# Kernel tuning notes

Measured on AMD Instinct MI355X. Metric: run time of the kernel, lower is better.

The kernel has to match this reference:

```python
import jax, jax.numpy as jnp
import numpy as np

D = 1024          # input_dim == output_dim (module requires this)
H = 4 * D         # expert hidden dim
E = 8             # num_experts
TOP_K = 2
N = 16384         # tokens


def setup_inputs() -> dict:
    key = jax.random.key(0)
    ks = jax.random.split(key, 8)
    s = 0.02
    return {
        "x": jax.random.normal(ks[0], (N, D), dtype=jnp.float32),
        "grad": jax.random.normal(ks[1], (N, 1), dtype=jnp.float32),
        "rW": jax.random.normal(ks[2], (D + 1, E), dtype=jnp.float32) * s,
        "rb": jnp.zeros((E,), dtype=jnp.float32),
        "W1": jax.random.normal(ks[3], (E, D, H), dtype=jnp.float32) * s,
        "b1": jnp.zeros((E, H), dtype=jnp.float32),
        "W2": jax.random.normal(ks[4], (E, H, D), dtype=jnp.float32) * s,
        "b2": jnp.zeros((E, D), dtype=jnp.float32),
    }


def reference(x, grad, rW, rb, W1, b1, W2, b2):
    # Router over [x, grad]
    logits = jnp.concatenate([x, grad], axis=-1) @ rW + rb          # [N, E]
    probs = jax.nn.softmax(logits, axis=-1)                          # [N, E]
    topk_probs, topk_idx = jax.lax.top_k(probs, TOP_K)               # [N, K]
    # Dense gate matrix: gate[n, e] = topk prob if e selected else 0
    gates = jnp.zeros_like(probs).at[jnp.arange(x.shape[0])[:, None], topk_idx].add(topk_probs)
    # Combine: out = sum_e gate_e * MLP_e(x). Dropout is identity at eval.
    out = jnp.zeros((x.shape[0], D), dtype=x.dtype)
    for e in range(E):  # fixed small loop over experts
        h = jax.nn.gelu(x @ W1[e] + b1[e], approximate=False)        # [N, H]
        y = h @ W2[e] + b2[e]                                        # [N, D]
        out = out + gates[:, e:e + 1] * y
    return out, probs
```

## Files before the change

kernel.cpp:

```cpp
#include <hip/hip_runtime.h>
#include <hip/hip_bf16.h>
#include <math.h>

#define NTOK 16384
#define DDIM 1024
#define HDIM 4096
#define NEXP 8

typedef __bf16 bf16_t;
typedef __bf16 bf16x8 __attribute__((ext_vector_type(8)));
typedef float f32x4 __attribute__((ext_vector_type(4)));

__device__ __forceinline__ void gld16(const bf16_t* g, bf16_t* l) {
    __builtin_amdgcn_global_load_lds(
        (const __attribute__((address_space(1))) void*)g,
        (__attribute__((address_space(3))) void*)l, 16, 0, 0);
}

__device__ __forceinline__ void stage_half(const bf16_t* __restrict__ g, int K, int kofs,
                                           bf16_t* l, int tid) {
#pragma unroll
    for (int c = 0; c < 2; ++c) {
        const int s = c * 512 + tid;
        const int kg = s >> 7, r = s & 127;
        gld16(g + (size_t)r * K + (kofs + kg * 8), l + (size_t)s * 8);
    }
}


__global__ void init_counts(int* counts) {
    if (threadIdx.x < NEXP) counts[threadIdx.x] = 0;
}

__global__ void router_kernel(const float* __restrict__ x, const float* __restrict__ grad,
                              const float* __restrict__ rW, const float* __restrict__ rb,
                              float* __restrict__ probs, int* __restrict__ t2i,
                              float* __restrict__ t2g, int* __restrict__ counts) {
    const int lane = threadIdx.x & 63;
    const int n = blockIdx.x * 4 + (threadIdx.x >> 6);
    float acc[NEXP];
#pragma unroll
    for (int e = 0; e < NEXP; ++e) acc[e] = 0.f;
    const float* xr = x + (size_t)n * DDIM;
    for (int d = lane; d < DDIM; d += 64) {
        float xv = xr[d];
        const float* rr = rW + (size_t)d * NEXP;
#pragma unroll
        for (int e = 0; e < NEXP; ++e) acc[e] = fmaf(xv, rr[e], acc[e]);
    }
#pragma unroll
    for (int e = 0; e < NEXP; ++e) {
#pragma unroll
        for (int off = 32; off > 0; off >>= 1)
            acc[e] += __shfl_xor(acc[e], off, 64);
    }
    if (lane == 0) {
        float gv = grad[n];
        float p[NEXP];
        float mx = -1e30f;
#pragma unroll
        for (int e = 0; e < NEXP; ++e) {
            p[e] = acc[e] + gv * rW[(size_t)DDIM * NEXP + e] + rb[e];
            mx = fmaxf(mx, p[e]);
        }
        float s = 0.f;
#pragma unroll
        for (int e = 0; e < NEXP; ++e) { p[e] = expf(p[e] - mx); s += p[e]; }
        float inv = 1.f / s;
        int i1 = 0; float v1 = -1.f;
#pragma unroll
        for (int e = 0; e < NEXP; ++e) {
            p[e] *= inv;
            probs[(size_t)n * NEXP + e] = p[e];
            if (p[e] > v1) { v1 = p[e]; i1 = e; }
        }
        int i2 = 0; float v2 = -2.f;
#pragma unroll
        for (int e = 0; e < NEXP; ++e) {
            if (e != i1 && p[e] > v2) { v2 = p[e]; i2 = e; }
        }
        t2i[n * 2] = i1; t2i[n * 2 + 1] = i2;
        t2g[n * 2] = v1; t2g[n * 2 + 1] = v2;
        atomicAdd(&counts[i1], 1);
        atomicAdd(&counts[i2], 1);
    }
}

__global__ void offsets_kernel(const int* __restrict__ counts, int* __restrict__ offsets,
                               int* __restrict__ cursor) {
    if (threadIdx.x == 0) {
        int s = 0;
        for (int e = 0; e < NEXP; ++e) { offsets[e] = s; cursor[e] = s; s += counts[e]; }
    }
}

__global__ void build_lists(const int* __restrict__ t2i, const float* __restrict__ t2g,
                            int* __restrict__ cursor, int* __restrict__ tok,
                            float* __restrict__ gate, int* __restrict__ tslot) {
    int n = blockIdx.x * 256 + threadIdx.x;
#pragma unroll
    for (int k = 0; k < 2; ++k) {
        int e = t2i[n * 2 + k];
        int slot = atomicAdd(&cursor[e], 1);
        tok[slot] = n;
        gate[slot] = t2g[n * 2 + k];
        tslot[n * 2 + k] = slot;
    }
}

__global__ void gather_kernel(const float* __restrict__ x, const int* __restrict__ tok,
                              bf16_t* __restrict__ Xg) {
    const int r = blockIdx.x;
    const int t = threadIdx.x;
    const int token = tok[r];
    float4 v = ((const float4*)(x + (size_t)token * DDIM))[t];
    bf16_t o[4] = { (bf16_t)v.x, (bf16_t)v.y, (bf16_t)v.z, (bf16_t)v.w };
    *(uint2*)(Xg + (size_t)r * DDIM + t * 4) = *(const uint2*)o;
}

__global__ void transpose_cast(const float* __restrict__ in, bf16_t* __restrict__ out,
                               int R, int C) {
    __shared__ float tile[32][33];
    const size_t ebase = (size_t)blockIdx.z * R * C;
    const int c0 = blockIdx.x * 32, r0 = blockIdx.y * 32;
    const int tx = threadIdx.x, ty = threadIdx.y;
#pragma unroll
    for (int j = 0; j < 32; j += 8)
        tile[ty + j][tx] = in[ebase + (size_t)(r0 + ty + j) * C + c0 + tx];
    __syncthreads();
#pragma unroll
    for (int j = 0; j < 32; j += 8)
        out[ebase + (size_t)(c0 + ty + j) * R + r0 + tx] = (bf16_t)tile[tx][ty + j];
}

__global__ void combine_kernel(const float* __restrict__ Yg, const int* __restrict__ tslot,
                               float* __restrict__ out) {
    const int n = blockIdx.x, t = threadIdx.x;
    const int s1 = tslot[n * 2], s2 = tslot[n * 2 + 1];
    const float4 a = ((const float4*)(Yg + (size_t)s1 * DDIM))[t];
    const float4 b = ((const float4*)(Yg + (size_t)s2 * DDIM))[t];
    ((float4*)(out + (size_t)n * DDIM))[t] =
        make_float4(a.x + b.x, a.y + b.y, a.z + b.z, a.w + b.w);
}

#define PHASE_SYNC() do { \
    __builtin_amdgcn_s_barrier(); \
    asm volatile("s_waitcnt lgkmcnt(0)" ::: "memory"); \
    __builtin_amdgcn_sched_barrier(0); \
    __builtin_amdgcn_s_setprio(1); \
} while (0)

#define PHASE_END() do { \
    __builtin_amdgcn_s_setprio(0); \
    __builtin_amdgcn_s_barrier(); \
} while (0)

#define MMA16(QA, QB) do { \
    _Pragma("unroll") \
    for (int mt = 0; mt < 4; ++mt) { \
        _Pragma("unroll") \
        for (int nt = 0; nt < 2; ++nt) { \
            _Pragma("unroll") \
            for (int ks = 0; ks < 2; ++ks) \
                acc[(QA) * 4 + mt][(QB) * 2 + nt] = \
                    __builtin_amdgcn_mfma_f32_16x16x32_bf16( \
                        aF[mt][ks], bF[nt][ks], acc[(QA) * 4 + mt][(QB) * 2 + nt], 0, 0, 0); \
        } \
    } \
} while (0)

template <int K, int EPI>
__global__ __launch_bounds__(512, 2)
void moe_gemm8(const bf16_t* __restrict__ A, const bf16_t* __restrict__ B,
               const float* __restrict__ bias, bf16_t* __restrict__ Hout,
               float* __restrict__ Yg, const int* __restrict__ counts,
               const int* __restrict__ offsets, const float* __restrict__ gate,
               int gx) {
    const int NT = K / 64;
    const int nwg = gridDim.x;
    const int q8 = nwg >> 3;
    const int v = (blockIdx.x & 7) * q8 + (blockIdx.x >> 3);
    const int per_e = gx * 64;
    const int e = v / per_e;
    const int rem = v - e * per_e;
    const int xsc = gx >> 2;
    const int sup = rem >> 5, sub = rem & 31;
    const int ys = sup / xsc, xs = sup - ys * xsc;
    const int yb = ys * 8 + (sub >> 2), xb = xs * 4 + (sub & 3);

    const int count = counts[e];
    const int m0 = yb * 256;
    if (m0 >= count) return;
    const int n0 = xb * 256;
    const int off = offsets[e];

    const bf16_t* Ae = A + (size_t)(off + m0) * K;
    const bf16_t* Be = B + (size_t)e * HDIM * DDIM + (size_t)n0 * K;
    const bf16_t* Ae1 = Ae + (size_t)128 * K;
    const bf16_t* Be1 = Be + (size_t)128 * K;

    __shared__ __align__(16) bf16_t lds[2][2][2][8192];

    const int tid = threadIdx.x;
    const int lane = tid & 63;
    const int lm = lane & 15, hi = lane >> 4;
    const int wv = tid >> 6;
    const int wm16 = (wv >> 2) << 4;
    const int wn16 = (wv & 3) << 4;

    f32x4 acc[8][4];
    const f32x4 zf = {0.f, 0.f, 0.f, 0.f};
#pragma unroll
    for (int i = 0; i < 8; ++i)
#pragma unroll
        for (int j = 0; j < 4; ++j) acc[i][j] = zf;

    bf16x8 aF[4][2], bF[2][2];
    auto readA = [&](const bf16_t* Ab) {
#pragma unroll
        for (int mt = 0; mt < 4; ++mt)
#pragma unroll
            for (int ks = 0; ks < 2; ++ks)
                aF[mt][ks] = *(const bf16x8*)(Ab + (size_t)((ks * 4 + hi) * 128 +
                                                            mt * 32 + wm16 + lm) * 8);
    };
    auto readB = [&](const bf16_t* Bb) {
#pragma unroll
        for (int nt = 0; nt < 2; ++nt)
#pragma unroll
            for (int ks = 0; ks < 2; ++ks)
                bF[nt][ks] = *(const bf16x8*)(Bb + (size_t)((ks * 4 + hi) * 128 +
                                                            nt * 64 + wn16 + lm) * 8);
    };

    stage_half(Ae,  K, 0, &lds[0][0][0][0], tid);
    stage_half(Ae1, K, 0, &lds[0][0][1][0], tid);
    stage_half(Be,  K, 0, &lds[0][1][0][0], tid);
    stage_half(Be1, K, 0, &lds[0][1][1][0], tid);
    const int k1p = (NT > 1 ? 1 : 0) * 64;
    stage_half(Ae,  K, k1p, &lds[1][0][0][0], tid);
    stage_half(Be1, K, k1p, &lds[1][1][1][0], tid);
    asm volatile("s_waitcnt vmcnt(4)" ::: "memory");
    __builtin_amdgcn_s_barrier();

    int cur = 0;
    for (int t = 0; t < NT; ++t, cur ^= 1) {
        const int nxt = cur ^ 1;
        const int k1 = ((t + 1 < NT) ? t + 1 : NT - 1) * 64;
        const int k2 = ((t + 2 < NT) ? t + 2 : NT - 1) * 64;
        readA(&lds[cur][0][0][0]);
        readB(&lds[cur][1][0][0]);
        stage_half(Ae1, K, k1, &lds[nxt][0][1][0], tid);
        stage_half(Be,  K, k1, &lds[nxt][1][0][0], tid);
        PHASE_SYNC(); MMA16(0, 0); PHASE_END();
        readB(&lds[cur][1][1][0]);
        stage_half(Ae, K, k2, &lds[cur][0][0][0], tid);
        PHASE_SYNC(); MMA16(0, 1); PHASE_END();
        readA(&lds[cur][0][1][0]);
        stage_half(Be1, K, k2, &lds[cur][1][1][0], tid);
        PHASE_SYNC(); MMA16(1, 1); PHASE_END();
        readB(&lds[cur][1][0][0]);
        PHASE_SYNC(); MMA16(1, 0);
        __builtin_amdgcn_s_setprio(0);
        asm volatile("s_waitcnt vmcnt(4)" ::: "memory");
        __builtin_amdgcn_s_barrier();
    }

    if (EPI == 0) {
        const float* bp = bias + (size_t)e * HDIM + n0;
#pragma unroll
        for (int mt = 0; mt < 8; ++mt) {
#pragma unroll
            for (int r = 0; r < 4; ++r) {
                const int row = m0 + mt * 32 + wm16 + hi * 4 + r;
                if (row < count) {
                    bf16_t* hrow = Hout + (size_t)(off + row) * HDIM + n0;
#pragma unroll
                    for (int nt = 0; nt < 4; ++nt) {
                        const int c = nt * 64 + wn16 + lm;
                        float vv = acc[mt][nt][r] + bp[c];
                        hrow[c] = (bf16_t)(0.5f * vv *
                                           (1.f + erff(vv * 0.70710678118654752f)));
                    }
                }
            }
        }
    } else {
        const float* bp = bias + (size_t)e * DDIM + n0;
#pragma unroll
        for (int mt = 0; mt < 8; ++mt) {
#pragma unroll
            for (int r = 0; r < 4; ++r) {
                const int row = m0 + mt * 32 + wm16 + hi * 4 + r;
                if (row < count) {
                    const int slot = off + row;
                    const float g = gate[slot];
                    float* yrow = Yg + (size_t)slot * DDIM + n0;
#pragma unroll
                    for (int nt = 0; nt < 4; ++nt) {
                        const int c = nt * 64 + wn16 + lm;
                        yrow[c] = g * (acc[mt][nt][r] + bp[c]);
                    }
                }
            }
        }
    }
}


extern "C" void kernel_launch(void* const* d_in, const int* in_sizes, int n_in,
                              void* d_out, int out_size, void* d_ws, size_t ws_size,
                              hipStream_t stream) {
    const float* x    = (const float*)d_in[0];
    const float* grad = (const float*)d_in[1];
    const float* rW   = (const float*)d_in[2];
    const float* rb   = (const float*)d_in[3];
    const float* W1   = (const float*)d_in[4];
    const float* b1   = (const float*)d_in[5];
    const float* W2   = (const float*)d_in[6];
    const float* b2   = (const float*)d_in[7];
    float* out   = (float*)d_out;
    float* probs = out + (size_t)NTOK * DDIM;

    char* base = (char*)d_ws;
    size_t p = 0;
    auto alloc = [&](size_t bytes) -> void* {
        void* r = base + p;
        p = (p + bytes + 255) & ~(size_t)255;
        return r;
    };

    int*    counts  = (int*)alloc(3 * NEXP * sizeof(int));
    int*    offsets = counts + NEXP;
    int*    cursor  = offsets + NEXP;
    int*    t2i   = (int*)alloc((size_t)NTOK * 2 * sizeof(int));
    float*  t2g   = (float*)alloc((size_t)NTOK * 2 * sizeof(float));
    int*    tok   = (int*)alloc((size_t)2 * NTOK * sizeof(int));
    float*  gate  = (float*)alloc((size_t)2 * NTOK * sizeof(float));
    int*    tslot = (int*)alloc((size_t)NTOK * 2 * sizeof(int));
    bf16_t* Xg   = (bf16_t*)alloc(((size_t)2 * NTOK + 256) * DDIM * sizeof(bf16_t));
    bf16_t* W1t  = (bf16_t*)alloc((size_t)NEXP * HDIM * DDIM * sizeof(bf16_t));
    bf16_t* W2t  = (bf16_t*)alloc((size_t)NEXP * HDIM * DDIM * sizeof(bf16_t));
    bf16_t* Hbuf = (bf16_t*)alloc(((size_t)2 * NTOK + 256) * HDIM * sizeof(bf16_t));
    float* Yg = (float*)Xg;

    hipLaunchKernelGGL(init_counts, dim3(1), dim3(64), 0, stream, counts);
    hipLaunchKernelGGL(router_kernel, dim3(NTOK / 4), dim3(256), 0, stream,
                       x, grad, rW, rb, probs, t2i, t2g, counts);
    hipLaunchKernelGGL(offsets_kernel, dim3(1), dim3(64), 0, stream, counts, offsets, cursor);
    hipLaunchKernelGGL(build_lists, dim3(NTOK / 256), dim3(256), 0, stream,
                       t2i, t2g, cursor, tok, gate, tslot);
    hipLaunchKernelGGL(gather_kernel, dim3(2 * NTOK), dim3(256), 0, stream, x, tok, Xg);
    hipLaunchKernelGGL(transpose_cast, dim3(HDIM / 32, DDIM / 32, NEXP), dim3(32, 8), 0, stream,
                       W1, W1t, DDIM, HDIM);
    hipLaunchKernelGGL(transpose_cast, dim3(DDIM / 32, HDIM / 32, NEXP), dim3(32, 8), 0, stream,
                       W2, W2t, HDIM, DDIM);

    hipLaunchKernelGGL((moe_gemm8<DDIM, 0>), dim3((HDIM / 256) * 64 * NEXP), dim3(512), 0,
                       stream, Xg, W1t, b1, Hbuf, (float*)nullptr, counts, offsets, gate,
                       HDIM / 256);
    hipLaunchKernelGGL((moe_gemm8<HDIM, 1>), dim3((DDIM / 256) * 64 * NEXP), dim3(512), 0,
                       stream, Hbuf, W2t, b2, (bf16_t*)nullptr, Yg, counts, offsets, gate,
                       DDIM / 256);
    hipLaunchKernelGGL(combine_kernel, dim3(NTOK), dim3(256), 0, stream, Yg, tslot, out);
}
```

Baseline: 2.062 ms.

## Restructure GEMM main loop to two-phase schedule and use fast erf approximation

The per-k-tile loop drops from four barrier-separated MMA phases to two. All A/B fragments for the tile are loaded from LDS up front into separate register arrays, and global-to-LDS staging is interleaved around a single mid-tile barrier. This removes several barriers per iteration but keeps more fragment registers live, which could pressure occupancy under launch_bounds(512,2). Separately, the GELU epilogue swaps erff for an Abramowitz-Stegun polynomial using rcp and expf to cut epilogue cost, at slightly lower accuracy.

```diff
diff --git a/kernel.cpp b/kernel.cpp
--- a/kernel.cpp
+++ b/kernel.cpp
@@ -25,6 +25,15 @@
         const int kg = s >> 7, r = s & 127;
         gld16(g + (size_t)r * K + (kofs + kg * 8), l + (size_t)s * 8);
     }
+}
+
+__device__ __forceinline__ float erf_fast(float u) {
+    float au = fabsf(u);
+    float tt = __builtin_amdgcn_rcpf(1.f + 0.3275911f * au);
+    float poly = tt * (0.254829592f + tt * (-0.284496736f +
+                 tt * (1.421413741f + tt * (-1.453152027f + tt * 1.061405429f))));
+    float er = 1.f - poly * __expf(-au * au);
+    return (u < 0.f) ? -er : er;
 }
 
 
@@ -143,19 +152,8 @@
         make_float4(a.x + b.x, a.y + b.y, a.z + b.z, a.w + b.w);
 }
 
-#define PHASE_SYNC() do { \
-    __builtin_amdgcn_s_barrier(); \
-    asm volatile("s_waitcnt lgkmcnt(0)" ::: "memory"); \
-    __builtin_amdgcn_sched_barrier(0); \
-    __builtin_amdgcn_s_setprio(1); \
-} while (0)
-
-#define PHASE_END() do { \
-    __builtin_amdgcn_s_setprio(0); \
-    __builtin_amdgcn_s_barrier(); \
-} while (0)
-
-#define MMA16(QA, QB) do { \
+
+#define MMA16Q(AF, BF, QA, QB) do { \
     _Pragma("unroll") \
     for (int mt = 0; mt < 4; ++mt) { \
         _Pragma("unroll") \
@@ -164,7 +162,7 @@
             for (int ks = 0; ks < 2; ++ks) \
                 acc[(QA) * 4 + mt][(QB) * 2 + nt] = \
                     __builtin_amdgcn_mfma_f32_16x16x32_bf16( \
-                        aF[mt][ks], bF[nt][ks], acc[(QA) * 4 + mt][(QB) * 2 + nt], 0, 0, 0); \
+                        AF[mt][ks], BF[nt][ks], acc[(QA) * 4 + mt][(QB) * 2 + nt], 0, 0, 0); \
         } \
     } \
 } while (0)
@@ -176,7 +174,7 @@
                float* __restrict__ Yg, const int* __restrict__ counts,
                const int* __restrict__ offsets, const float* __restrict__ gate,
                int gx) {
-    const int NT = K / 64;
+    constexpr int NT = K / 64;
     const int nwg = gridDim.x;
     const int q8 = nwg >> 3;
     const int v = (blockIdx.x & 7) * q8 + (blockIdx.x >> 3);
@@ -215,22 +213,21 @@
 #pragma unroll
         for (int j = 0; j < 4; ++j) acc[i][j] = zf;
 
-    bf16x8 aF[4][2], bF[2][2];
-    auto readA = [&](const bf16_t* Ab) {
+    auto readA = [&](bf16x8 (&d)[4][2], const bf16_t* Ab) {
 #pragma unroll
         for (int mt = 0; mt < 4; ++mt)
 #pragma unroll
             for (int ks = 0; ks < 2; ++ks)
-                aF[mt][ks] = *(const bf16x8*)(Ab + (size_t)((ks * 4 + hi) * 128 +
-                                                            mt * 32 + wm16 + lm) * 8);
+                d[mt][ks] = *(const bf16x8*)(Ab + (size_t)((ks * 4 + hi) * 128 +
+                                                           mt * 32 + wm16 + lm) * 8);
     };
-    auto readB = [&](const bf16_t* Bb) {
+    auto readB = [&](bf16x8 (&d)[2][2], const bf16_t* Bb) {
 #pragma unroll
         for (int nt = 0; nt < 2; ++nt)
 #pragma unroll
             for (int ks = 0; ks < 2; ++ks)
-                bF[nt][ks] = *(const bf16x8*)(Bb + (size_t)((ks * 4 + hi) * 128 +
-                                                            nt * 64 + wn16 + lm) * 8);
+                d[nt][ks] = *(const bf16x8*)(Bb + (size_t)((ks * 4 + hi) * 128 +
+                                                           nt * 64 + wn16 + lm) * 8);
     };
 
     stage_half(Ae,  K, 0, &lds[0][0][0][0], tid);
@@ -242,28 +239,36 @@
     stage_half(Be1, K, k1p, &lds[1][1][1][0], tid);
     asm volatile("s_waitcnt vmcnt(4)" ::: "memory");
     __builtin_amdgcn_s_barrier();
-
-    int cur = 0;
-    for (int t = 0; t < NT; ++t, cur ^= 1) {
-        const int nxt = cur ^ 1;
-        const int k1 = ((t + 1 < NT) ? t + 1 : NT - 1) * 64;
-        const int k2 = ((t + 2 < NT) ? t + 2 : NT - 1) * 64;
-        readA(&lds[cur][0][0][0]);
-        readB(&lds[cur][1][0][0]);
-        stage_half(Ae1, K, k1, &lds[nxt][0][1][0], tid);
-        stage_half(Be,  K, k1, &lds[nxt][1][0][0], tid);
-        PHASE_SYNC(); MMA16(0, 0); PHASE_END();
-        readB(&lds[cur][1][1][0]);
-        stage_half(Ae, K, k2, &lds[cur][0][0][0], tid);
-        PHASE_SYNC(); MMA16(0, 1); PHASE_END();
-        readA(&lds[cur][0][1][0]);
-        stage_half(Be1, K, k2, &lds[cur][1][1][0], tid);
-        PHASE_SYNC(); MMA16(1, 1); PHASE_END();
-        readB(&lds[cur][1][0][0]);
-        PHASE_SYNC(); MMA16(1, 0);
+    __builtin_amdgcn_sched_barrier(0);
+
+    for (int t = 0; t < NT; ++t) {
+        const int c = t & 1, nx = c ^ 1;
+        const int kS1 = ((t + 1 < NT) ? t + 1 : NT - 1) * 64;
+        const int kS2 = ((t + 2 < NT) ? t + 2 : NT - 1) * 64;
+
+        bf16x8 a0[4][2], a1[4][2], b0[2][2], b1[2][2];
+        readA(a0, &lds[c][0][0][0]);
+        readB(b0, &lds[c][1][0][0]);
+        readB(b1, &lds[c][1][1][0]);
+        readA(a1, &lds[c][0][1][0]);
+        stage_half(Ae1, K, kS1, &lds[nx][0][1][0], tid);
+        stage_half(Be,  K, kS1, &lds[nx][1][0][0], tid);
+        __builtin_amdgcn_sched_barrier(0);
+        __builtin_amdgcn_s_setprio(1);
+        MMA16Q(a0, b0, 0, 0);
+        MMA16Q(a0, b1, 0, 1);
+        asm volatile("s_waitcnt lgkmcnt(0)" ::: "memory");
+        __builtin_amdgcn_s_barrier();
+        __builtin_amdgcn_sched_barrier(0);
+        stage_half(Ae,  K, kS2, &lds[c][0][0][0], tid);
+        stage_half(Be1, K, kS2, &lds[c][1][1][0], tid);
+        __builtin_amdgcn_sched_barrier(0);
+        MMA16Q(a1, b1, 1, 1);
+        MMA16Q(a1, b0, 1, 0);
         __builtin_amdgcn_s_setprio(0);
         asm volatile("s_waitcnt vmcnt(4)" ::: "memory");
         __builtin_amdgcn_s_barrier();
+        __builtin_amdgcn_sched_barrier(0);
     }
 
     if (EPI == 0) {
@@ -277,10 +282,10 @@
                     bf16_t* hrow = Hout + (size_t)(off + row) * HDIM + n0;
 #pragma unroll
                     for (int nt = 0; nt < 4; ++nt) {
-                        const int c = nt * 64 + wn16 + lm;
-                        float vv = acc[mt][nt][r] + bp[c];
-                        hrow[c] = (bf16_t)(0.5f * vv *
-                                           (1.f + erff(vv * 0.70710678118654752f)));
+                        const int cc = nt * 64 + wn16 + lm;
+                        float vv = acc[mt][nt][r] + bp[cc];
+                        float er = erf_fast(vv * 0.70710678118654752f);
+                        hrow[cc] = (bf16_t)(0.5f * vv * (1.f + er));
                     }
                 }
             }
@@ -298,8 +303,8 @@
                     float* yrow = Yg + (size_t)slot * DDIM + n0;
 #pragma unroll
                     for (int nt = 0; nt < 4; ++nt) {
-                        const int c = nt * 64 + wn16 + lm;
-                        yrow[c] = g * (acc[mt][nt][r] + bp[c]);
+                        const int cc = nt * 64 + wn16 + lm;
+                        yrow[cc] = g * (acc[mt][nt][r] + bp[cc]);
                     }
                 }
             }
```

Result: slower. 2.165 ms (+5.0%).
